# Kernel tuning notes

Hardware: AMD Instinct MI355X
Metric: run time of the kernel (lower is better)

## Reference

```python
import jax, jax.numpy as jnp
import numpy as np

NUM_HEADS = 16
HEAD_DIM = 128
HIDDEN = NUM_HEADS * HEAD_DIM  # 2048
ROPE_BASE = 10000.0


def _rope_tables(seq_len, dtype=jnp.float32):
    inv_freq = 1.0 / (ROPE_BASE ** (jnp.arange(0, HEAD_DIM, 2, dtype=jnp.float32) / HEAD_DIM))
    freqs = jnp.arange(seq_len, dtype=jnp.float32)[:, None] * inv_freq[None, :]  # [S, hd/2]
    return jnp.cos(freqs).astype(dtype), jnp.sin(freqs).astype(dtype)


def _apply_rope(x, cos, sin):
    # x: [B, S, H, hd]; interleaved even/odd rotation
    B, S, H, D = x.shape
    xr = x.reshape(B, S, H, D // 2, 2)
    x_even, x_odd = xr[..., 0], xr[..., 1]
    c = cos[None, :, None, :]
    s = sin[None, :, None, :]
    rot_even = x_even * c - x_odd * s
    rot_odd = x_even * s + x_odd * c
    return jnp.stack([rot_even, rot_odd], axis=-1).reshape(B, S, H, D)


def setup_inputs() -> dict:
    key = jax.random.key(0)
    k1, k2, k3, k4, k5 = jax.random.split(key, 5)
    B, S = 2, 2048
    hidden_states = jax.random.normal(k1, (B, S, HIDDEN), dtype=jnp.float32)
    attention_mask = jnp.zeros((B, 1, 1, S), dtype=jnp.float32)
    scale = 1.0 / np.sqrt(HIDDEN)
    Wqkv = jax.random.normal(k2, (3 * HIDDEN, HIDDEN), dtype=jnp.float32) * scale
    bqkv = jnp.zeros((3 * HIDDEN,), dtype=jnp.float32)
    Wout = jax.random.normal(k3, (HIDDEN, HIDDEN), dtype=jnp.float32) * scale
    bout = jnp.zeros((HIDDEN,), dtype=jnp.float32)
    return {"hidden_states": hidden_states, "attention_mask": attention_mask,
            "Wqkv": Wqkv, "bqkv": bqkv, "Wout": Wout, "bout": bout}


def reference(hidden_states, attention_mask, Wqkv, bqkv, Wout, bout):
    B, S, _ = hidden_states.shape
    scale = 1.0 / np.sqrt(HEAD_DIM)
    qkv = hidden_states @ Wqkv.T + bqkv                      # [B, S, 3*HIDDEN]
    qkv = qkv.reshape(B, S, 3, NUM_HEADS, HEAD_DIM)
    q, k, v = qkv[:, :, 0], qkv[:, :, 1], qkv[:, :, 2]       # [B, S, H, hd]
    cos, sin = _rope_tables(S, hidden_states.dtype)
    q = _apply_rope(q, cos, sin)
    k = _apply_rope(k, cos, sin)
    scores = jnp.einsum('bqhd,bkhd->bhqk', q, k) * scale     # [B, H, S, S]
    scores = scores + attention_mask
    probs = jax.nn.softmax(scores, axis=-1)
    ctx = jnp.einsum('bhqk,bkhd->bqhd', probs, v)            # [B, S, H, hd]
    ctx = ctx.reshape(B, S, HIDDEN)
    return ctx @ Wout.T + bout
```

## Files before the change

kernel.cpp:

```cpp
#include <hip/hip_runtime.h>
#include <math.h>

#define HID    2048
#define NH     16
#define HD     128
#define SEQ    2048
#define NBATCH 2
#define NT     (SEQ / 64)

typedef __attribute__((ext_vector_type(8))) short bf16x8;
typedef __attribute__((ext_vector_type(4))) float f32x4;

__device__ __forceinline__ short f2bf(float f) {
    union { float f; unsigned u; } x; x.f = f;
    unsigned r = x.u + 0x7fffu + ((x.u >> 16) & 1u);
    return (short)(r >> 16);
}
__device__ __forceinline__ float bf2f(short s) {
    union { unsigned u; float f; } y;
    y.u = ((unsigned)(unsigned short)s) << 16;
    return y.f;
}

__device__ __forceinline__ void gl_lds16(const short* g, short* l) {
    __builtin_amdgcn_global_load_lds(
        (const __attribute__((address_space(1))) unsigned int*)g,
        (__attribute__((address_space(3))) unsigned int*)l, 16, 0, 0);
}

__global__ __launch_bounds__(256) void rope_table_kernel(float2* __restrict__ cst) {
    int idx = blockIdx.x * 256 + threadIdx.x;
    if (idx >= SEQ * 64) return;
    int s = idx >> 6;
    int i = idx & 63;
    double inv = pow(10000.0, -(double)i / 64.0);
    float freq = (float)s * (float)inv;
    float2 cs = make_float2(cosf(freq), sinf(freq));
    cst[s * HD + 2 * i]     = cs;
    cst[s * HD + 2 * i + 1] = cs;
}

__global__ __launch_bounds__(256) void split_h_kernel(const float* __restrict__ in,
                                                      short* __restrict__ oh, int n4) {
    int i = blockIdx.x * 256 + threadIdx.x;
    if (i >= n4) return;
    float4 v = ((const float4*)in)[i];
    short4 h;
    h.x = f2bf(v.x); h.y = f2bf(v.y); h.z = f2bf(v.z); h.w = f2bf(v.w);
    *(short4*)(oh + 4 * (size_t)i) = h;
}

#define LDSA 0
#define LDSB 4096

template <int MODE>
__global__ __launch_bounds__(256, 3) void gemm_bf16_kernel(
    const short* __restrict__ Ah, const short* __restrict__ Bh,
    const float* __restrict__ bias, float* __restrict__ C,
    short* __restrict__ qb, short* __restrict__ kbf, short* __restrict__ vTt,
    const float2* __restrict__ cst) {
    __shared__ short lds[MODE == 0 ? 18432 : 8192];

    const int t     = threadIdx.x;
    const int w     = t >> 6;
    const int lane  = t & 63;
    const int mfrag = lane & 15;
    const int quad  = lane >> 4;
    const int wm    = (w >> 1) * 64;
    const int wn    = (w & 1) * 64;
    const int m0    = blockIdx.y * 128;
    const int n0    = blockIdx.x * 128;

    const int srow   = lane >> 2;
    const int schunk = (((lane & 3) ^ ((lane >> 3) & 3))) * 8;
    const short* gA0 = Ah + (size_t)(m0 + w * 16 + srow) * HID + schunk;
    const short* gA1 = Ah + (size_t)(m0 + 64 + w * 16 + srow) * HID + schunk;
    const short* gB0 = Bh + (size_t)(n0 + w * 16 + srow) * HID + schunk;
    const short* gB1 = Bh + (size_t)(n0 + 64 + w * 16 + srow) * HID + schunk;
    short* lA0 = &lds[LDSA + (w * 16) * 32];
    short* lA1 = &lds[LDSA + (64 + w * 16) * 32];
    short* lB0 = &lds[LDSB + (w * 16) * 32];
    short* lB1 = &lds[LDSB + (64 + w * 16) * 32];

    const int chA = 8 * (quad ^ ((mfrag >> 1) & 3));

    f32x4 acc[4][4];
#pragma unroll
    for (int i = 0; i < 4; ++i)
#pragma unroll
        for (int j = 0; j < 4; ++j) acc[i][j] = (f32x4){0.f, 0.f, 0.f, 0.f};

    for (int kt = 0; kt < HID; kt += 32) {
        __syncthreads();
        gl_lds16(gA0 + kt, lA0);
        gl_lds16(gA1 + kt, lA1);
        gl_lds16(gB0 + kt, lB0);
        gl_lds16(gB1 + kt, lB1);
        __syncthreads();

        bf16x8 ah[4], bh[4];
#pragma unroll
        for (int mt = 0; mt < 4; ++mt)
            ah[mt] = *(const bf16x8*)&lds[LDSA + (wm + mt * 16 + mfrag) * 32 + chA];
#pragma unroll
        for (int nt = 0; nt < 4; ++nt)
            bh[nt] = *(const bf16x8*)&lds[LDSB + (wn + nt * 16 + mfrag) * 32 + chA];

#pragma unroll
        for (int mt = 0; mt < 4; ++mt)
#pragma unroll
            for (int nt = 0; nt < 4; ++nt)
                acc[mt][nt] = __builtin_amdgcn_mfma_f32_16x16x32_bf16(
                    ah[mt], bh[nt], acc[mt][nt], 0, 0, 0);
    }

    float bcol[4];
#pragma unroll
    for (int nt = 0; nt < 4; ++nt) bcol[nt] = bias[n0 + wn + nt * 16 + mfrag];

    if (MODE == 0) {
        const int which = n0 >> 11;
        const int h     = (n0 & 2047) >> 7;
        const int bidx  = m0 >> 11;
        if (which < 2) {
            short* dst = (which == 0) ? qb : kbf;
            const float post = (which == 0) ? 0.08838834764831845f : 1.0f;
#pragma unroll
            for (int mt = 0; mt < 4; ++mt)
#pragma unroll
                for (int r = 0; r < 4; ++r) {
                    int sl = (m0 & 2047) + wm + mt * 16 + 4 * quad + r;
                    const float2* csr = cst + (size_t)sl * HD;
#pragma unroll
                    for (int nt = 0; nt < 4; ++nt) {
                        float x  = acc[mt][nt][r] + bcol[nt];
                        float px = __shfl_xor(x, 1, 64);
                        int   d  = wn + nt * 16 + mfrag;
                        float2 cs = csr[d];
                        float rot = (mfrag & 1) ? fmaf(px, cs.y, x * cs.x)
                                                : (x * cs.x - px * cs.y);
                        dst[((size_t)(bidx * NH + h) * SEQ + sl) * HD + d] =
                            f2bf(rot * post);
                    }
                }
        } else {
            __syncthreads();
            short* tw = &lds[w * 4608];
#pragma unroll
            for (int mt = 0; mt < 4; ++mt)
#pragma unroll
                for (int nt = 0; nt < 4; ++nt)
#pragma unroll
                    for (int r = 0; r < 4; ++r)
                        tw[(nt * 16 + mfrag) * 72 + (mt * 16 + 4 * quad + r)] =
                            f2bf(acc[mt][nt][r] + bcol[nt]);
            const size_t vbase = (size_t)(bidx * NH + h) * HD * SEQ;
            const int sbase = (m0 & 2047) + wm;
#pragma unroll
            for (int it = 0; it < 8; ++it) {
                int dl  = it * 8 + (lane >> 3);
                int cch = (lane & 7) ^ (lane >> 3);
                bf16x8 row = *(const bf16x8*)&tw[dl * 72 + cch * 8];
                *(bf16x8*)(vTt + vbase + (size_t)(wn + dl) * SEQ + sbase + cch * 8) = row;
            }
        }
    } else {
#pragma unroll
        for (int mt = 0; mt < 4; ++mt)
#pragma unroll
            for (int r = 0; r < 4; ++r) {
                int m = m0 + wm + mt * 16 + 4 * quad + r;
#pragma unroll
                for (int nt = 0; nt < 4; ++nt)
                    C[(size_t)m * HID + n0 + wn + nt * 16 + mfrag] =
                        acc[mt][nt][r] + bcol[nt];
            }
    }
}

#define AK0 0
#define AK1 8192
#define AV0 16384
#define AV1 24576
#define AP  32768

__global__ __launch_bounds__(512, 4) void attn_mfma_kernel(
    const short* __restrict__ qb, const short* __restrict__ kbf,
    const short* __restrict__ vTt, const float* __restrict__ mask,
    short* __restrict__ ctxb) {
    __shared__ __align__(16) short lds[40960];

    const int t    = threadIdx.x;
    const int w    = t >> 6;
    const int lane = t & 63;
    const int m    = lane & 15;
    const int quad = lane >> 4;

    const int id  = blockIdx.x;
    const int j   = id >> 3;
    const int bh  = (id & 7) * 4 + (j >> 4);
    const int q0  = (j & 15) * 128;
    const int b   = bh >> 4;
    const int h   = bh & 15;

    const size_t base = (size_t)bh * SEQ * HD;
    const short* kp = kbf + base;
    const short* vp = vTt + base;
    const float* mrow = mask + (size_t)b * SEQ;

    size_t kOff[2], vOff[2];
    int kDst[2], vDst[2];
#pragma unroll
    for (int u = 0; u < 2; ++u) {
        int rk = w * 8 + u * 4 + (lane >> 4);
        int ck = (lane & 15) ^ (rk & 7);
        kOff[u] = (size_t)rk * HD + ck * 8;
        kDst[u] = (w * 8 + u * 4) * 128;
        int rv = w * 16 + u * 8 + (lane >> 3);
        int cv = (lane & 7) ^ (rv & 7);
        vOff[u] = (size_t)rv * SEQ + cv * 8;
        vDst[u] = (w * 16 + u * 8) * 64;
    }

    const int srow = q0 + w * 16 + m;
    bf16x8 qh[4];
    {
        const short* qhp = qb + base + (size_t)srow * HD;
#pragma unroll
        for (int c = 0; c < 4; ++c)
            qh[c] = *(const bf16x8*)(qhp + 32 * c + 8 * quad);
    }

    f32x4 O[8];
    float m_i[4], l_p[4];
#pragma unroll
    for (int c = 0; c < 8; ++c) O[c] = (f32x4){0.f, 0.f, 0.f, 0.f};
#pragma unroll
    for (int r = 0; r < 4; ++r) { m_i[r] = -INFINITY; l_p[r] = 0.f; }

    const int sw = m & 7;
    const int pb = AP + w * 1024;
    const int kcb = (m >> 3);
    const int ml  = m & 7;

#pragma unroll
    for (int u = 0; u < 2; ++u) {
        gl_lds16(kp + kOff[u], &lds[AK0 + kDst[u]]);
        gl_lds16(vp + vOff[u], &lds[AV0 + vDst[u]]);
    }

    for (int kt = 0; kt < NT; ++kt) {
        const int cur = kt & 1;
        const int k0  = kt * 64;

        __syncthreads();

        if (kt + 1 < NT) {
            const int nk0 = (kt + 1) * 64;
            const int nb  = cur ^ 1;
#pragma unroll
            for (int u = 0; u < 2; ++u) {
                gl_lds16(kp + (size_t)nk0 * HD + kOff[u],
                         &lds[(nb ? AK1 : AK0) + kDst[u]]);
                gl_lds16(vp + nk0 + vOff[u],
                         &lds[(nb ? AV1 : AV0) + vDst[u]]);
            }
        }

        const short* kb = &lds[cur ? AK1 : AK0];
        const short* vb = &lds[cur ? AV1 : AV0];

        float mk[4];
#pragma unroll
        for (int c2 = 0; c2 < 4; ++c2) mk[c2] = mrow[k0 + 16 * c2 + m];

        f32x4 S[4];
        __builtin_amdgcn_s_setprio(1);
#pragma unroll
        for (int c2 = 0; c2 < 4; ++c2) {
            f32x4 acc = (f32x4){0.f, 0.f, 0.f, 0.f};
#pragma unroll
            for (int c = 0; c < 4; ++c) {
                int pk = (4 * c + quad) ^ sw;
                bf16x8 kf = *(const bf16x8*)&kb[(16 * c2 + m) * 128 + pk * 8];
                acc = __builtin_amdgcn_mfma_f32_16x16x32_bf16(qh[c], kf, acc, 0, 0, 0);
            }
            S[c2] = acc;
        }
        __builtin_amdgcn_s_setprio(0);

        float rm4[4];
#pragma unroll
        for (int r = 0; r < 4; ++r) {
            float s0 = S[0][r] + mk[0];
            float s1 = S[1][r] + mk[1];
            float s2 = S[2][r] + mk[2];
            float s3 = S[3][r] + mk[3];
            S[0][r] = s0; S[1][r] = s1; S[2][r] = s2; S[3][r] = s3;
            float rm = fmaxf(fmaxf(s0, s1), fmaxf(s2, s3));
#pragma unroll
            for (int off = 1; off < 16; off <<= 1)
                rm = fmaxf(rm, __shfl_xor(rm, off, 64));
            rm4[r] = rm;
        }
        int needI = (rm4[0] > m_i[0] + 8.f) | (rm4[1] > m_i[1] + 8.f) |
                    (rm4[2] > m_i[2] + 8.f) | (rm4[3] > m_i[3] + 8.f);
        if (__any(needI)) {
#pragma unroll
            for (int r = 0; r < 4; ++r) {
                float mn = fmaxf(m_i[r], rm4[r]);
                float a  = __expf(m_i[r] - mn);
                m_i[r]   = mn;
                l_p[r]  *= a;
#pragma unroll
                for (int c = 0; c < 8; ++c) O[c][r] *= a;
            }
        }
        float p[4][4];
#pragma unroll
        for (int r = 0; r < 4; ++r) {
#pragma unroll
            for (int c2 = 0; c2 < 4; ++c2) p[c2][r] = __expf(S[c2][r] - m_i[r]);
            l_p[r] += (p[0][r] + p[1][r]) + (p[2][r] + p[3][r]);
        }

#pragma unroll
        for (int c2 = 0; c2 < 4; ++c2) {
#pragma unroll
            for (int jj = 0; jj < 2; ++jj) {
                unsigned pkw;
                asm("v_cvt_pk_bf16_f32 %0, %1, %2"
                    : "=v"(pkw) : "v"(p[c2][2 * jj]), "v"(p[c2][2 * jj + 1]));
                int ql = 4 * quad + 2 * jj;
                int qh2 = ql + 1;
                lds[pb + ql * 64 + (((2 * c2 + kcb) ^ (ql & 7)) << 3) + ml] =
                    (short)(pkw & 0xffffu);
                lds[pb + qh2 * 64 + (((2 * c2 + kcb) ^ (qh2 & 7)) << 3) + ml] =
                    (short)(pkw >> 16);
            }
        }

        __builtin_amdgcn_s_setprio(1);
#pragma unroll
        for (int cc = 0; cc < 2; ++cc) {
            int pv = (4 * cc + quad) ^ sw;
            bf16x8 pf = *(const bf16x8*)&lds[pb + m * 64 + (pv << 3)];
#pragma unroll
            for (int c = 0; c < 8; ++c) {
                bf16x8 vf = *(const bf16x8*)&vb[(16 * c + m) * 64 + pv * 8];
                O[c] = __builtin_amdgcn_mfma_f32_16x16x32_bf16(pf, vf, O[c], 0, 0, 0);
            }
        }
        __builtin_amdgcn_s_setprio(0);
    }

#pragma unroll
    for (int r = 0; r < 4; ++r) {
        float lv = l_p[r];
#pragma unroll
        for (int off = 1; off < 16; off <<= 1) lv += __shfl_xor(lv, off, 64);
        float inv = 1.0f / lv;
        int s = q0 + w * 16 + 4 * quad + r;
        size_t off2 = ((size_t)(b * SEQ + s)) * HID + h * HD;
#pragma unroll
        for (int c = 0; c < 8; ++c)
            ctxb[off2 + 16 * c + m] = f2bf(O[c][r] * inv);
    }
}

extern "C" void kernel_launch(void* const* d_in, const int* in_sizes, int n_in,
                              void* d_out, int out_size, void* d_ws, size_t ws_size,
                              hipStream_t stream) {
    const float* hs   = (const float*)d_in[0];
    const float* mask = (const float*)d_in[1];
    const float* Wqkv = (const float*)d_in[2];
    const float* bqkv = (const float*)d_in[3];
    const float* Wout = (const float*)d_in[4];
    const float* bout = (const float*)d_in[5];
    float* out = (float*)d_out;

    const size_t qkv_elems = (size_t)NBATCH * NH * SEQ * HD;
    char* p = (char*)d_ws;
    float2* cst  = (float2*)p; p += (size_t)SEQ * HD * 8;
    short* qbf   = (short*)p; p += qkv_elems * 2;
    short* kbf   = (short*)p; p += qkv_elems * 2;
    short* vTt   = (short*)p; p += qkv_elems * 2;
    short* Wqkvh = (short*)p; p += (size_t)3 * HID * HID * 2;
    short* Wouth = (short*)p; p += (size_t)HID * HID * 2;
    short* Ahs   = (short*)p; p += qkv_elems * 2;
    short* ctxb  = Ahs;

    rope_table_kernel<<<(SEQ * 64 + 255) / 256, 256, 0, stream>>>(cst);

    split_h_kernel<<<(int)(qkv_elems / 4 / 256), 256, 0, stream>>>(
        hs, Ahs, (int)(qkv_elems / 4));
    split_h_kernel<<<(int)((size_t)3 * HID * HID / 4 / 256), 256, 0, stream>>>(
        Wqkv, Wqkvh, (int)((size_t)3 * HID * HID / 4));
    split_h_kernel<<<(int)((size_t)HID * HID / 4 / 256), 256, 0, stream>>>(
        Wout, Wouth, (int)((size_t)HID * HID / 4));

    gemm_bf16_kernel<0><<<dim3(48, 32), 256, 0, stream>>>(
        Ahs, Wqkvh, bqkv, nullptr, qbf, kbf, vTt, cst);

    attn_mfma_kernel<<<512, 512, 0, stream>>>(qbf, kbf, vTt, mask, ctxb);

    gemm_bf16_kernel<1><<<dim3(16, 32), 256, 0, stream>>>(
        ctxb, Wouth, bout, out, nullptr, nullptr, nullptr, nullptr);
}
```

Measured before the change: 422.2 us.

## Replace QKV GEMM with 256x256-tile double-buffered kernel with priority scheduling

```diff
diff --git a/kernel.cpp b/kernel.cpp
--- a/kernel.cpp
+++ b/kernel.cpp
@@ -53,13 +53,10 @@
 #define LDSA 0
 #define LDSB 4096
 
-template <int MODE>
-__global__ __launch_bounds__(256, 3) void gemm_bf16_kernel(
+__global__ __launch_bounds__(256, 3) void gemm_out_kernel(
     const short* __restrict__ Ah, const short* __restrict__ Bh,
-    const float* __restrict__ bias, float* __restrict__ C,
-    short* __restrict__ qb, short* __restrict__ kbf, short* __restrict__ vTt,
-    const float2* __restrict__ cst) {
-    __shared__ short lds[MODE == 0 ? 18432 : 8192];
+    const float* __restrict__ bias, float* __restrict__ C) {
+    __shared__ short lds[8192];
 
     const int t     = threadIdx.x;
     const int w     = t >> 6;
@@ -118,63 +115,164 @@
 #pragma unroll
     for (int nt = 0; nt < 4; ++nt) bcol[nt] = bias[n0 + wn + nt * 16 + mfrag];
 
-    if (MODE == 0) {
-        const int which = n0 >> 11;
-        const int h     = (n0 & 2047) >> 7;
-        const int bidx  = m0 >> 11;
-        if (which < 2) {
-            short* dst = (which == 0) ? qb : kbf;
-            const float post = (which == 0) ? 0.08838834764831845f : 1.0f;
-#pragma unroll
-            for (int mt = 0; mt < 4; ++mt)
+#pragma unroll
+    for (int mt = 0; mt < 4; ++mt)
+#pragma unroll
+        for (int r = 0; r < 4; ++r) {
+            int mm = m0 + wm + mt * 16 + 4 * quad + r;
+#pragma unroll
+            for (int nt = 0; nt < 4; ++nt)
+                C[(size_t)mm * HID + n0 + wn + nt * 16 + mfrag] =
+                    acc[mt][nt][r] + bcol[nt];
+        }
+}
+
+#define PR1 __builtin_amdgcn_s_setprio(1)
+#define PR0 __builtin_amdgcn_s_setprio(0)
+#define BARX __builtin_amdgcn_s_barrier()
+#define LGKM0 { asm volatile("s_waitcnt lgkmcnt(0)" ::: "memory"); \
+                __builtin_amdgcn_sched_barrier(0); }
+#define VMC(n) asm volatile("s_waitcnt vmcnt(" #n ")" ::: "memory")
+
+#define STAGE_A(bf, ke) { _Pragma("unroll") for (int c = 0; c < 4; ++c) \
+    gl_lds16(Ag + (size_t)(c * 64) * HID + (ke), &lds[(bf) * 32768 + sdst + c * 4096]); }
+#define STAGE_B(bf, ke) { _Pragma("unroll") for (int c = 0; c < 4; ++c) \
+    gl_lds16(Bg + (size_t)(c * 64) * HID + (ke), &lds[(bf) * 32768 + 16384 + sdst + c * 4096]); }
+
+#define LOADA(bf, mh) { _Pragma("unroll") for (int x = 0; x < 4; ++x) { \
+    aF[x][0] = *(const bf16x8*)&lds[(bf) * 32768 + aoff + ((mh) * 4 + x) * 1024 + fc0]; \
+    aF[x][1] = *(const bf16x8*)&lds[(bf) * 32768 + aoff + ((mh) * 4 + x) * 1024 + fc1]; } }
+#define LOADB(bf, nh, dstF) { _Pragma("unroll") for (int x = 0; x < 2; ++x) { \
+    dstF[x][0] = *(const bf16x8*)&lds[(bf) * 32768 + 16384 + boff + ((nh) * 2 + x) * 1024 + fc0]; \
+    dstF[x][1] = *(const bf16x8*)&lds[(bf) * 32768 + 16384 + boff + ((nh) * 2 + x) * 1024 + fc1]; } }
+#define QUADM(mh, nh, bF) { _Pragma("unroll") for (int x = 0; x < 4; ++x) \
+    _Pragma("unroll") for (int y = 0; y < 2; ++y) { \
+    acc[(mh) * 4 + x][(nh) * 2 + y] = __builtin_amdgcn_mfma_f32_16x16x32_bf16( \
+        aF[x][0], bF[y][0], acc[(mh) * 4 + x][(nh) * 2 + y], 0, 0, 0); \
+    acc[(mh) * 4 + x][(nh) * 2 + y] = __builtin_amdgcn_mfma_f32_16x16x32_bf16( \
+        aF[x][1], bF[y][1], acc[(mh) * 4 + x][(nh) * 2 + y], 0, 0, 0); } }
+
+__global__ __launch_bounds__(512, 2) void gemm256_qkv_kernel(
+    const short* __restrict__ Ah, const short* __restrict__ Bh,
+    const float* __restrict__ bias,
+    short* __restrict__ qb, short* __restrict__ kbf, short* __restrict__ vTt,
+    const float2* __restrict__ cst) {
+    __shared__ __align__(16) short lds[65536];
+
+    const int t    = threadIdx.x;
+    const int w    = t >> 6;
+    const int lane = t & 63;
+    const int m    = lane & 15;
+    const int quad = lane >> 4;
+    const int wm   = w >> 2;
+    const int wn   = w & 3;
+
+    const int swz = (blockIdx.x & 7) * 48 + (blockIdx.x >> 3);
+    const int bx  = swz / 16;
+    const int by  = swz % 16;
+    const int m0  = by * 256;
+    const int n0  = bx * 256;
+
+    const int srl = lane >> 3;
+    const int sch = ((lane & 7) ^ (srl & 7)) * 8;
+    const short* Ag = Ah + (size_t)(m0 + w * 8 + srl) * HID + sch;
+    const short* Bg = Bh + (size_t)(n0 + w * 8 + srl) * HID + sch;
+    const int sdst  = w * 512;
+
+    const int key  = m & 7;
+    const int fc0  = (quad ^ key) * 8;
+    const int fc1  = ((4 + quad) ^ key) * 8;
+    const int aoff = (wm * 128 + m) * 64;
+    const int boff = (wn * 64 + m) * 64;
+
+    f32x4 acc[8][4];
+#pragma unroll
+    for (int i = 0; i < 8; ++i)
+#pragma unroll
+        for (int j = 0; j < 4; ++j) acc[i][j] = (f32x4){0.f, 0.f, 0.f, 0.f};
+
+    bf16x8 aF[4][2], b0F[2][2], b1F[2][2];
+
+    STAGE_A(0, 0); STAGE_B(0, 0);
+    STAGE_A(1, 64); STAGE_B(1, 64);
+    VMC(8); BARX;
+
+    const int NIT = HID / 128;
+#pragma unroll 1
+    for (int i = 0; i < NIT; ++i) {
+        const int keN = (i + 1) * 128;
+        LOADA(0, 0); LOADB(0, 0, b0F);
+        if (i) STAGE_B(1, i * 128 + 64);
+        BARX; LGKM0; PR1; QUADM(0, 0, b0F); PR0; BARX;
+        LOADB(0, 1, b1F);
+        BARX; LGKM0; PR1; QUADM(0, 1, b1F); PR0; BARX;
+        LOADA(0, 1);
+        BARX; LGKM0; PR1; QUADM(1, 1, b1F); PR0; BARX;
+        if (i + 1 < NIT) { STAGE_A(0, keN); VMC(4); } else { VMC(0); }
+        BARX; PR1; QUADM(1, 0, b0F); PR0; BARX;
+        LOADA(1, 0); LOADB(1, 0, b0F);
+        if (i + 1 < NIT) STAGE_B(0, keN);
+        BARX; LGKM0; PR1; QUADM(0, 0, b0F); PR0; BARX;
+        LOADB(1, 1, b1F);
+        BARX; LGKM0; PR1; QUADM(0, 1, b1F); PR0; BARX;
+        LOADA(1, 1);
+        BARX; LGKM0; PR1; QUADM(1, 1, b1F); PR0; BARX;
+        if (i + 1 < NIT) { STAGE_A(1, keN + 64); VMC(4); }
+        BARX; PR1; QUADM(1, 0, b0F); PR0; BARX;
+    }
+
+    const int which = n0 >> 11;
+    const int bidx  = m0 >> 11;
+    const int cb    = (n0 & 2047) + wn * 64;
+    const int h     = cb >> 7;
+    const int d0    = cb & 127;
+
+    float bcol[4];
+#pragma unroll
+    for (int nt = 0; nt < 4; ++nt) bcol[nt] = bias[n0 + wn * 64 + nt * 16 + m];
+
+    if (which < 2) {
+        short* dst = (which == 0) ? qb : kbf;
+        const float post = (which == 0) ? 0.08838834764831845f : 1.0f;
+#pragma unroll
+        for (int mt = 0; mt < 8; ++mt)
+#pragma unroll
+            for (int r = 0; r < 4; ++r) {
+                int sl = (m0 & 2047) + wm * 128 + mt * 16 + 4 * quad + r;
+                const float2* csr = cst + (size_t)sl * HD;
+                size_t rowb = ((size_t)(bidx * NH + h) * SEQ + sl) * HD;
+#pragma unroll
+                for (int nt = 0; nt < 4; ++nt) {
+                    float x  = acc[mt][nt][r] + bcol[nt];
+                    float px = __shfl_xor(x, 1, 64);
+                    int   d  = d0 + nt * 16 + m;
+                    float2 cs = csr[d];
+                    float rot = (m & 1) ? fmaf(px, cs.y, x * cs.x)
+                                        : (x * cs.x - px * cs.y);
+                    dst[rowb + d] = f2bf(rot * post);
+                }
+            }
+    } else {
+        short* tw = &lds[w * 8192];
+#pragma unroll
+        for (int mt = 0; mt < 8; ++mt)
+#pragma unroll
+            for (int nt = 0; nt < 4; ++nt)
 #pragma unroll
                 for (int r = 0; r < 4; ++r) {
-                    int sl = (m0 & 2047) + wm + mt * 16 + 4 * quad + r;
-                    const float2* csr = cst + (size_t)sl * HD;
-#pragma unroll
-                    for (int nt = 0; nt < 4; ++nt) {
-                        float x  = acc[mt][nt][r] + bcol[nt];
-                        float px = __shfl_xor(x, 1, 64);
-                        int   d  = wn + nt * 16 + mfrag;
-                        float2 cs = csr[d];
-                        float rot = (mfrag & 1) ? fmaf(px, cs.y, x * cs.x)
-                                                : (x * cs.x - px * cs.y);
-                        dst[((size_t)(bidx * NH + h) * SEQ + sl) * HD + d] =
-                            f2bf(rot * post);
-                    }
+                    int s_l = mt * 16 + 4 * quad + r;
+                    int d_l = nt * 16 + m;
+                    tw[d_l * 128 + (((s_l >> 3) ^ m) << 3) + (s_l & 7)] =
+                        f2bf(acc[mt][nt][r] + bcol[nt]);
                 }
-        } else {
-            __syncthreads();
-            short* tw = &lds[w * 4608];
-#pragma unroll
-            for (int mt = 0; mt < 4; ++mt)
-#pragma unroll
-                for (int nt = 0; nt < 4; ++nt)
-#pragma unroll
-                    for (int r = 0; r < 4; ++r)
-                        tw[(nt * 16 + mfrag) * 72 + (mt * 16 + 4 * quad + r)] =
-                            f2bf(acc[mt][nt][r] + bcol[nt]);
-            const size_t vbase = (size_t)(bidx * NH + h) * HD * SEQ;
-            const int sbase = (m0 & 2047) + wm;
-#pragma unroll
-            for (int it = 0; it < 8; ++it) {
-                int dl  = it * 8 + (lane >> 3);
-                int cch = (lane & 7) ^ (lane >> 3);
-                bf16x8 row = *(const bf16x8*)&tw[dl * 72 + cch * 8];
-                *(bf16x8*)(vTt + vbase + (size_t)(wn + dl) * SEQ + sbase + cch * 8) = row;
-            }
-        }
-    } else {
-#pragma unroll
-        for (int mt = 0; mt < 4; ++mt)
-#pragma unroll
-            for (int r = 0; r < 4; ++r) {
-                int m = m0 + wm + mt * 16 + 4 * quad + r;
-#pragma unroll
-                for (int nt = 0; nt < 4; ++nt)
-                    C[(size_t)m * HID + n0 + wn + nt * 16 + mfrag] =
-                        acc[mt][nt][r] + bcol[nt];
-            }
+        const size_t vbase = (size_t)(bidx * NH + h) * HD * SEQ;
+        const int sbase = (m0 & 2047) + wm * 128;
+#pragma unroll
+        for (int it = 0; it < 16; ++it) {
+            int d_l = it * 4 + quad;
+            bf16x8 row = *(const bf16x8*)&tw[d_l * 128 + ((m ^ (d_l & 15)) << 3)];
+            *(bf16x8*)(vTt + vbase + (size_t)(d0 + d_l) * SEQ + sbase + m * 8) = row;
+        }
     }
 }
 
@@ -399,11 +497,10 @@
     split_h_kernel<<<(int)((size_t)HID * HID / 4 / 256), 256, 0, stream>>>(
         Wout, Wouth, (int)((size_t)HID * HID / 4));
 
-    gemm_bf16_kernel<0><<<dim3(48, 32), 256, 0, stream>>>(
-        Ahs, Wqkvh, bqkv, nullptr, qbf, kbf, vTt, cst);
+    gemm256_qkv_kernel<<<384, 512, 0, stream>>>(
+        Ahs, Wqkvh, bqkv, qbf, kbf, vTt, cst);
 
     attn_mfma_kernel<<<512, 512, 0, stream>>>(qbf, kbf, vTt, mask, ctxb);
 
-    gemm_bf16_kernel<1><<<dim3(16, 32), 256, 0, stream>>>(
-        ctxb, Wouth, bout, out, nullptr, nullptr, nullptr, nullptr);
-}
+    gemm_out_kernel<<<dim3(16, 32), 256, 0, stream>>>(ctxb, Wouth, bout, out);
+}
```

Result: no change. 422.8 us (+0.1%).
